# Performance work log

Hardware: AMD Instinct MI355X
Metric: run time of the kernel (lower is better)

Reference implementation:

```python
import jax, jax.numpy as jnp
import numpy as np

N, E, G = 50000, 800000, 500
F_IN, H_DIM, L, NH, HD, OUT = 74, 256, 4, 8, 32, 1
SLOPE, EPS = 0.2, 1e-5


def setup_inputs() -> dict:
    key = jax.random.key(0)
    ks = jax.random.split(key, 24)
    rn = lambda k, s, sc: jax.random.normal(k, s, jnp.float32) * sc
    inp = {
        "x": jax.random.normal(ks[0], (N, F_IN), jnp.float32),
        "edge_index": jax.random.randint(ks[1], (2, E), 0, N),
        "batch": jnp.sort(jax.random.randint(ks[2], (N,), 0, G)),
        "in_w": rn(ks[3], (F_IN, H_DIM), 1.0 / np.sqrt(F_IN)),
        "in_b": jnp.zeros((H_DIM,), jnp.float32),
        "wl": rn(ks[4], (L, H_DIM, H_DIM), 1.0 / np.sqrt(H_DIM)),
        "wl_b": jnp.zeros((L, H_DIM), jnp.float32),
        "wr": rn(ks[5], (L, H_DIM, H_DIM), 1.0 / np.sqrt(H_DIM)),
        "wr_b": jnp.zeros((L, H_DIM), jnp.float32),
        "att": rn(ks[6], (L, NH, HD), 1.0 / np.sqrt(HD)),
        "gat_b": jnp.zeros((L, H_DIM), jnp.float32),
        "ln_g": jnp.ones((L, H_DIM), jnp.float32),
        "ln_b": jnp.zeros((L, H_DIM), jnp.float32),
        "out_w": rn(ks[7], (H_DIM, H_DIM), 1.0 / np.sqrt(H_DIM)),
        "out_b": jnp.zeros((H_DIM,), jnp.float32),
        "p1_w": rn(ks[8], (H_DIM, H_DIM // 2), 1.0 / np.sqrt(H_DIM)),
        "p1_b": jnp.zeros((H_DIM // 2,), jnp.float32),
        "bn1_g": jnp.ones((H_DIM // 2,), jnp.float32),
        "bn1_b": jnp.zeros((H_DIM // 2,), jnp.float32),
        "p2_w": rn(ks[9], (H_DIM // 2, H_DIM // 4), 1.0 / np.sqrt(H_DIM // 2)),
        "p2_b": jnp.zeros((H_DIM // 4,), jnp.float32),
        "bn2_g": jnp.ones((H_DIM // 4,), jnp.float32),
        "bn2_b": jnp.zeros((H_DIM // 4,), jnp.float32),
        "p3_w": rn(ks[10], (H_DIM // 4, OUT), 1.0 / np.sqrt(H_DIM // 4)),
        "p3_b": jnp.zeros((OUT,), jnp.float32),
    }
    return inp


def _layer_norm(x, g, b):
    m = x.mean(-1, keepdims=True)
    v = ((x - m) ** 2).mean(-1, keepdims=True)
    return (x - m) * jax.lax.rsqrt(v + EPS) * g + b


def _batch_norm(x, g, b):
    m = x.mean(0)
    v = ((x - m) ** 2).mean(0)
    return (x - m) * jax.lax.rsqrt(v + EPS) * g + b


def _gatv2(h, src, dst, wl, wl_b, wr, wr_b, att, bias, n):
    xl = (h @ wl + wl_b).reshape(n, NH, HD)  # source transform
    xr = (h @ wr + wr_b).reshape(n, NH, HD)  # target transform
    e = jax.nn.leaky_relu(xl[src] + xr[dst], SLOPE)      # [E, H, D]
    score = jnp.einsum('ehd,hd->eh', e, att)             # [E, H]
    smax = jax.ops.segment_max(score, dst, num_segments=n)
    num = jnp.exp(score - smax[dst])
    den = jax.ops.segment_sum(num, dst, num_segments=n)
    alpha = num / (den[dst] + 1e-16)                     # segment softmax per dst
    out = jax.ops.segment_sum(xl[src] * alpha[:, :, None], dst, num_segments=n)
    return out.reshape(n, NH * HD) + bias


def reference(x, edge_index, batch, in_w, in_b, wl, wl_b, wr, wr_b, att, gat_b,
              ln_g, ln_b, out_w, out_b, p1_w, p1_b, bn1_g, bn1_b,
              p2_w, p2_b, bn2_g, bn2_b, p3_w, p3_b):
    n = x.shape[0]
    loops = jnp.arange(n)
    src = jnp.concatenate([edge_index[0], loops])  # add self-loops (PyG default)
    dst = jnp.concatenate([edge_index[1], loops])
    h = x @ in_w + in_b
    for i in range(L):
        res = h
        g = _gatv2(h, src, dst, wl[i], wl_b[i], wr[i], wr_b[i], att[i], gat_b[i], n)
        if i > 0:
            g = g + res
        h = jax.nn.relu(_layer_norm(g, ln_g[i], ln_b[i]))
    h = h @ out_w + out_b
    cnt = jax.ops.segment_sum(jnp.ones((n,), h.dtype), batch, num_segments=G)
    gr = jax.ops.segment_sum(h, batch, num_segments=G) / jnp.maximum(cnt, 1.0)[:, None]
    z = jax.nn.relu(_batch_norm(gr @ p1_w + p1_b, bn1_g, bn1_b))
    z = jax.nn.relu(_batch_norm(z @ p2_w + p2_b, bn2_g, bn2_b))
    return z @ p3_w + p3_b
```

## Files before the change

### kernel.cpp

```cpp
#include <hip/hip_runtime.h>
#include <hip/hip_bf16.h>

#define F_IN   74
#define KPAD   96
#define HDIM   256
#define NHEAD  8
#define HEADD  32
#define NLAYER 4
#define SLOPE  0.2f
#define EPSN   1e-5f
#define LOG2E  1.44269504088896f

typedef __attribute__((ext_vector_type(8))) short bf16x8;
typedef __attribute__((ext_vector_type(4))) float f32x4;
typedef __attribute__((ext_vector_type(2))) float f32x2;

__device__ __forceinline__ float bf2f(unsigned short u){
  union { unsigned int i; float f; } x; x.i = ((unsigned int)u) << 16; return x.f;
}
__device__ __forceinline__ unsigned short f2bf(float f){
  union { float f; unsigned int i; } x; x.f = f;
  unsigned int u = x.i;
  return (unsigned short)((u + 0x7FFFu + ((u >> 16) & 1u)) >> 16);
}
__device__ __forceinline__ f32x2 bfpair(unsigned int u){
  union { unsigned int i; float f; } lo, hi;
  lo.i = u << 16; hi.i = u & 0xffff0000u;
  return (f32x2){lo.f, hi.f};
}
__device__ __forceinline__ float dpp_sum8(float p){
  int t;
  t = __builtin_amdgcn_update_dpp(0, __float_as_int(p), 0xB1, 0xF, 0xF, true);
  p += __int_as_float(t);
  t = __builtin_amdgcn_update_dpp(0, __float_as_int(p), 0x4E, 0xF, 0xF, true);
  p += __int_as_float(t);
  t = __builtin_amdgcn_update_dpp(0, __float_as_int(p), 0x141, 0xF, 0xF, true);
  p += __int_as_float(t);
  return p;
}
__device__ __forceinline__ float dpp_sum16(float p){
  int t;
  p = dpp_sum8(p);
  t = __builtin_amdgcn_update_dpp(0, __float_as_int(p), 0x140, 0xF, 0xF, true);
  p += __int_as_float(t);
  return p;
}

#define GLOAD16(g, s) __builtin_amdgcn_global_load_lds( \
  (const __attribute__((address_space(1))) void*)(g), \
  (__attribute__((address_space(3))) void*)(s), 16, 0, 0)

__global__ void k_hist(const int* __restrict__ dst, int* __restrict__ deg, int e){
  int i = blockIdx.x * 256 + threadIdx.x;
  if (i < e) atomicAdd(&deg[dst[i]], 1);
}

__global__ __launch_bounds__(256) void k_scan1(const int* __restrict__ deg,
    int* __restrict__ rowp, int* __restrict__ bsum, int n){
  __shared__ int wsum[4];
  const int tid = threadIdx.x, lane = tid & 63, wid = tid >> 6;
  const int i = blockIdx.x * 256 + tid;
  int v = (i < n) ? (deg[i] + 1) : 0;
  int xv = v;
  #pragma unroll
  for (int off = 1; off < 64; off <<= 1){
    int t = __shfl_up(xv, off);
    if (lane >= off) xv += t;
  }
  if (lane == 63) wsum[wid] = xv;
  __syncthreads();
  int woff = 0, total = 0;
  #pragma unroll
  for (int w = 0; w < 4; ++w){
    int s = wsum[w];
    total += s;
    if (w < wid) woff += s;
  }
  if (i < n) rowp[i] = woff + xv - v;
  if (tid == 0) bsum[blockIdx.x] = total;
}
__global__ __launch_bounds__(256) void k_scan2(const int* __restrict__ bsum,
    int* __restrict__ boff, int nb){
  __shared__ int wsum[4];
  const int tid = threadIdx.x, lane = tid & 63, wid = tid >> 6;
  int v = (tid < nb) ? bsum[tid] : 0;
  int xv = v;
  #pragma unroll
  for (int off = 1; off < 64; off <<= 1){
    int t = __shfl_up(xv, off);
    if (lane >= off) xv += t;
  }
  if (lane == 63) wsum[wid] = xv;
  __syncthreads();
  int woff = 0, total = 0;
  #pragma unroll
  for (int w = 0; w < 4; ++w){
    int s = wsum[w];
    total += s;
    if (w < wid) woff += s;
  }
  if (tid <= nb) boff[tid] = woff + xv - v;
  if (tid == 0) boff[nb] = total;
}
__global__ void k_scan3(int* __restrict__ rowp, int* __restrict__ cur,
                        const int* __restrict__ boff, int n, int nb){
  int i = blockIdx.x * 256 + threadIdx.x;
  if (i < n){
    int v = rowp[i] + boff[blockIdx.x];
    rowp[i] = v;
    cur[i] = v;
  }
  if (i == 0) rowp[n] = boff[nb];
}

__global__ void k_fill2(const int* __restrict__ src, const int* __restrict__ dst,
                        int* __restrict__ cur, unsigned int* __restrict__ csr,
                        int e, int n){
  int i = blockIdx.x * 256 + threadIdx.x;
  if (i < e){
    int p = atomicAdd(&cur[dst[i]], 1);
    csr[p] = ((unsigned int)src[i]) << 10;
  } else if (i < e + n){
    int v = i - e;
    int p = atomicAdd(&cur[v], 1);
    csr[p] = ((unsigned int)v) << 10;
  }
}

__global__ __launch_bounds__(256) void k_prep(
    const float* __restrict__ wl, const float* __restrict__ wr,
    const float* __restrict__ out_w, const float* __restrict__ in_w,
    const float* __restrict__ wl_b, const float* __restrict__ wr_b,
    const float* __restrict__ x,
    unsigned short* __restrict__ WtLR, unsigned short* __restrict__ WtO,
    unsigned short* __restrict__ WtI, float* __restrict__ bconc,
    unsigned short* __restrict__ xb, int n)
{
  const int b = blockIdx.x;
  const int tid = threadIdx.x;
  if (b < 576){
    __shared__ float tile[32][33];
    const float* Wm;
    unsigned short* Wo;
    int rem, colbase;
    if (b < 512){
      const int matset = b >> 8;
      const int mat = (b >> 6) & 3;
      rem = b & 63;
      const float* srcw = matset ? wr : wl;
      Wm = srcw + (size_t)mat * HDIM * HDIM;
      Wo = WtLR + (size_t)mat * 512 * HDIM;
      colbase = matset * 256;
    } else {
      rem = b - 512;
      Wm = out_w; Wo = WtO; colbase = 0;
    }
    const int c0 = (rem & 7) * 32, r0 = (rem >> 3) * 32;
    const int tx = tid & 31, ty = tid >> 5;
    #pragma unroll
    for (int i = 0; i < 32; i += 8)
      tile[ty + i][tx] = Wm[(size_t)(r0 + ty + i) * HDIM + c0 + tx];
    __syncthreads();
    #pragma unroll
    for (int i = 0; i < 32; i += 8){
      const int col = colbase + c0 + ty + i;
      const int k   = r0 + tx;
      const int cb = col >> 4, ks = k >> 5;
      const int lf = (col & 15) | (((k >> 3) & 3) << 4);
      Wo[((size_t)(cb * 8 + ks) * 64 + lf) * 8 + (k & 7)] = f2bf(tile[tx][ty + i]);
    }
  } else if (b < 672){
    int idx = (b - 576) * 256 + tid;
    int c = idx / KPAD, k = idx - c * KPAD;
    float v = (k < F_IN) ? in_w[(size_t)k * HDIM + c] : 0.f;
    WtI[idx] = f2bf(v);
  } else if (b < 680){
    int i = (b - 672) * 256 + tid;
    if (i < NLAYER * 512){
      int layer = i >> 9, c = i & 511;
      bconc[i] = (c < 256) ? wl_b[layer * 256 + c] : wr_b[layer * 256 + (c - 256)];
    }
  } else {
    int idx = (b - 680) * 256 + tid;
    if (idx < n * KPAD){
      int row = idx / KPAD, k = idx - row * KPAD;
      float v = (k < F_IN) ? x[(size_t)row * F_IN + k] : 0.f;
      xb[idx] = f2bf(v);
    }
  }
}

__global__ __launch_bounds__(256) void k_inproj_mfma(
    const unsigned short* __restrict__ xb, const unsigned short* __restrict__ Wt,
    const float* __restrict__ bias, unsigned short* __restrict__ C, int M)
{
  const int l = threadIdx.x & 63;
  const int w = threadIdx.x >> 6;
  const int wm = w >> 1, wn = w & 1;
  const int row0 = blockIdx.x * 128;
  const int col0 = blockIdx.y * 128;

  f32x4 acc[4][4];
  #pragma unroll
  for (int i = 0; i < 4; ++i)
    #pragma unroll
    for (int j = 0; j < 4; ++j) acc[i][j] = (f32x4){0.f, 0.f, 0.f, 0.f};

  #pragma unroll
  for (int kk = 0; kk < 3; ++kk){
    const int kof = kk * 32 + (l >> 4) * 8;
    bf16x8 af[4], bfr[4];
    #pragma unroll
    for (int mi = 0; mi < 4; ++mi){
      int row = row0 + wm * 64 + mi * 16 + (l & 15);
      if (row > M - 1) row = M - 1;
      af[mi] = *(const bf16x8*)(xb + (size_t)row * KPAD + kof);
    }
    #pragma unroll
    for (int ni = 0; ni < 4; ++ni){
      const int col = col0 + wn * 64 + ni * 16 + (l & 15);
      bfr[ni] = *(const bf16x8*)(Wt + (size_t)col * KPAD + kof);
    }
    #pragma unroll
    for (int mi = 0; mi < 4; ++mi)
      #pragma unroll
      for (int ni = 0; ni < 4; ++ni)
        acc[mi][ni] = __builtin_amdgcn_mfma_f32_16x16x32_bf16(
            af[mi], bfr[ni], acc[mi][ni], 0, 0, 0);
  }

  #pragma unroll
  for (int mi = 0; mi < 4; ++mi){
    #pragma unroll
    for (int ni = 0; ni < 4; ++ni){
      const int col = col0 + wn * 64 + ni * 16 + (l & 15);
      const float bv = bias[col];
      #pragma unroll
      for (int r = 0; r < 4; ++r){
        const int row = row0 + wm * 64 + mi * 16 + (l >> 4) * 4 + r;
        if (row < M) C[(size_t)row * HDIM + col] = f2bf(acc[mi][ni][r] + bv);
      }
    }
  }
}

__global__ __launch_bounds__(256) void k_gemm_mfma(
    const unsigned short* __restrict__ A, const unsigned short* __restrict__ Wt,
    const float* __restrict__ bias, unsigned short* __restrict__ C, int M, int ldc)
{
  __shared__ unsigned short As[2][128 * 64];
  const int tid = threadIdx.x;
  const int l   = tid & 63;
  const int w   = tid >> 6;
  const int wm  = w >> 1, wn = w & 1;
  const int row0 = blockIdx.x * 128;
  const int col0 = blockIdx.y * 128;

  const int srow   = l >> 3;
  const int schunk = l & 7;

  f32x4 acc[4][4];
  #pragma unroll
  for (int i = 0; i < 4; ++i)
    #pragma unroll
    for (int j = 0; j < 4; ++j) acc[i][j] = (f32x4){0.f, 0.f, 0.f, 0.f};

  auto stageA = [&](int buf, int k0){
    #pragma unroll
    for (int i = 0; i < 4; ++i){
      const int rloc = w * 32 + i * 8 + srow;
      const int sw   = (schunk ^ (rloc & 7)) * 16;
      int ra = row0 + rloc; if (ra > M - 1) ra = M - 1;
      const char* srcA = (const char*)(A + (size_t)ra * HDIM + k0) + sw;
      GLOAD16(srcA, &As[buf][(w * 32 + i * 8) * 64]);
    }
  };

  const unsigned short* Bf = Wt + ((size_t)(col0 / 16 + wn * 4) * 8 * 64 + l) * 8;

  stageA(0, 0);
  asm volatile("s_waitcnt vmcnt(0)" ::: "memory");
  __builtin_amdgcn_s_barrier();
  int buf = 0;
  #pragma unroll
  for (int t = 0; t < 4; ++t){
    bf16x8 bfr[2][4];
    #pragma unroll
    for (int kk = 0; kk < 2; ++kk)
      #pragma unroll
      for (int ni = 0; ni < 4; ++ni)
        bfr[kk][ni] = *(const bf16x8*)(Bf + ((size_t)ni * 8 + (t * 2 + kk)) * 64 * 8);
    if (t < 3) stageA(buf ^ 1, (t + 1) * 64);
    #pragma unroll
    for (int kk = 0; kk < 2; ++kk){
      bf16x8 af[4];
      #pragma unroll
      for (int mi = 0; mi < 4; ++mi){
        const int row = wm * 64 + mi * 16 + (l & 15);
        const int tt  = (kk * 4 + (l >> 4)) ^ (row & 7);
        af[mi] = *(const bf16x8*)((const char*)&As[buf][0] + row * 128 + tt * 16);
      }
      #pragma unroll
      for (int mi = 0; mi < 4; ++mi)
        #pragma unroll
        for (int ni = 0; ni < 4; ++ni)
          acc[mi][ni] = __builtin_amdgcn_mfma_f32_16x16x32_bf16(
              af[mi], bfr[kk][ni], acc[mi][ni], 0, 0, 0);
    }
    if (t < 3){
      asm volatile("s_waitcnt vmcnt(0)" ::: "memory");
      __builtin_amdgcn_s_barrier();
      buf ^= 1;
    }
  }

  #pragma unroll
  for (int mi = 0; mi < 4; ++mi){
    #pragma unroll
    for (int ni = 0; ni < 4; ++ni){
      const int col = col0 + wn * 64 + ni * 16 + (l & 15);
      const float bv = bias[col];
      #pragma unroll
      for (int r = 0; r < 4; ++r){
        const int row = row0 + wm * 64 + mi * 16 + (l >> 4) * 4 + r;
        if (row < M) C[(size_t)row * ldc + col] = f2bf(acc[mi][ni][r] + bv);
      }
    }
  }
}

__global__ __launch_bounds__(256) void k_gat(
    const unsigned short* __restrict__ xlr,
    const int* __restrict__ rp, const unsigned int* __restrict__ csr,
    const float* __restrict__ att, const float* __restrict__ gb,
    const float* __restrict__ lg, const float* __restrict__ lb,
    const unsigned short* __restrict__ hold, unsigned short* __restrict__ hnew,
    int n, int use_res)
{
  const int node = blockIdx.x * 4 + (threadIdx.x >> 6);
  if (node >= n) return;
  const int lane = threadIdx.x & 63;
  const int elem = lane << 2;
  const int head = lane >> 3;
  float4 attv = *(const float4*)(att + head * HEADD + (elem & 31));
  const f32x2 av01 = {attv.x * LOG2E, attv.y * LOG2E};
  const f32x2 av23 = {attv.z * LOG2E, attv.w * LOG2E};
  uint2 ur = *(const uint2*)(xlr + (size_t)node * 512 + 256 + elem);
  const f32x2 r01 = bfpair(ur.x), r23 = bfpair(ur.y);

  const char* xbase = (const char*)xlr + (elem << 1);

  f32x2 a01 = {0.f, 0.f}, a23 = {0.f, 0.f};
  float l = 0.f;

  auto edgeq = [&](uint2 uu, f32x2& x01, f32x2& x23)->float{
    x01 = bfpair(uu.x); x23 = bfpair(uu.y);
    f32x2 t01 = x01 + r01, t23 = x23 + r23;
    f32x2 m01 = __builtin_elementwise_max(t01, t01 * SLOPE);
    f32x2 m23 = __builtin_elementwise_max(t23, t23 * SLOPE);
    f32x2 d = m01 * av01 + m23 * av23;
    float p = dpp_sum8(d.x + d.y);
    return exp2f(p);
  };

  const int e0 = rp[node], e1 = rp[node + 1];
  int e = e0;
  for (; e + 4 <= e1; e += 4){
    unsigned int o0 = csr[e], o1 = csr[e + 1], o2 = csr[e + 2], o3 = csr[e + 3];
    uint2 u0 = *(const uint2*)(xbase + o0);
    uint2 u1 = *(const uint2*)(xbase + o1);
    uint2 u2 = *(const uint2*)(xbase + o2);
    uint2 u3 = *(const uint2*)(xbase + o3);
    f32x2 x01, x23;
    float q0 = edgeq(u0, x01, x23);
    a01 += q0 * x01; a23 += q0 * x23;
    float q1 = edgeq(u1, x01, x23);
    a01 += q1 * x01; a23 += q1 * x23;
    float q2 = edgeq(u2, x01, x23);
    a01 += q2 * x01; a23 += q2 * x23;
    float q3 = edgeq(u3, x01, x23);
    a01 += q3 * x01; a23 += q3 * x23;
    l += (q0 + q1) + (q2 + q3);
  }
  for (; e < e1; ++e){
    unsigned int o = csr[e];
    uint2 u = *(const uint2*)(xbase + o);
    f32x2 x01, x23;
    float q = edgeq(u, x01, x23);
    l += q;
    a01 += q * x01; a23 += q * x23;
  }

  const float inv = 1.f / l;
  const size_t base = (size_t)node * HDIM + elem;
  float f0 = a01.x * inv + gb[elem + 0];
  float f1 = a01.y * inv + gb[elem + 1];
  float f2 = a23.x * inv + gb[elem + 2];
  float f3 = a23.y * inv + gb[elem + 3];
  if (use_res){
    ushort4 hv = *(const ushort4*)(hold + base);
    f0 += bf2f(hv.x); f1 += bf2f(hv.y); f2 += bf2f(hv.z); f3 += bf2f(hv.w);
  }
  float s = f0 + f1 + f2 + f3;
  s = dpp_sum16(s);
  s += __shfl_xor(s, 16);
  s += __shfl_xor(s, 32);
  const float mean = s * (1.f / HDIM);
  float d0 = f0 - mean, d1 = f1 - mean, d2 = f2 - mean, d3 = f3 - mean;
  float q = d0 * d0 + d1 * d1 + d2 * d2 + d3 * d3;
  q = dpp_sum16(q);
  q += __shfl_xor(q, 16);
  q += __shfl_xor(q, 32);
  const float rs = rsqrtf(q * (1.f / HDIM) + EPSN);
  float o0 = d0 * rs * lg[elem + 0] + lb[elem + 0]; o0 = o0 > 0.f ? o0 : 0.f;
  float o1 = d1 * rs * lg[elem + 1] + lb[elem + 1]; o1 = o1 > 0.f ? o1 : 0.f;
  float o2 = d2 * rs * lg[elem + 2] + lb[elem + 2]; o2 = o2 > 0.f ? o2 : 0.f;
  float o3 = d3 * rs * lg[elem + 3] + lb[elem + 3]; o3 = o3 > 0.f ? o3 : 0.f;
  ushort4 st; st.x = f2bf(o0); st.y = f2bf(o1); st.z = f2bf(o2); st.w = f2bf(o3);
  *(ushort4*)(hnew + base) = st;
}

__global__ __launch_bounds__(256) void k_pool2(
    const unsigned short* __restrict__ ho, const int* __restrict__ batch,
    float* __restrict__ gr, int n)
{
  const int g = blockIdx.x;
  int lo = 0, hi = n;
  while (lo < hi){ int mid = (lo + hi) >> 1; if (batch[mid] < g) lo = mid + 1; else hi = mid; }
  const int s = lo;
  hi = n;
  while (lo < hi){ int mid = (lo + hi) >> 1; if (batch[mid] < g + 1) lo = mid + 1; else hi = mid; }
  const int e = lo;
  const int j = threadIdx.x;
  float acc = 0.f;
  for (int i = s; i < e; ++i) acc += bf2f(ho[(size_t)i * HDIM + j]);
  int c = e - s; if (c < 1) c = 1;
  gr[(size_t)g * HDIM + j] = acc / (float)c;
}

__global__ void k_fc(const float* __restrict__ in, const float* __restrict__ w,
                     const float* __restrict__ b, float* __restrict__ out,
                     int kin, int kout){
  __shared__ float s[256];
  int g = blockIdx.x, j = threadIdx.x;
  for (int k = j; k < kin; k += blockDim.x) s[k] = in[(size_t)g * kin + k];
  __syncthreads();
  float a = b[j];
  for (int k = 0; k < kin; ++k) a = fmaf(s[k], w[k * kout + j], a);
  out[(size_t)g * kout + j] = a;
}

__global__ __launch_bounds__(256) void k_bn(float* __restrict__ z,
    const float* __restrict__ gam, const float* __restrict__ bet, int g_, int c_){
  const int c = blockIdx.x;
  float s = 0.f, s2 = 0.f;
  for (int r = threadIdx.x; r < g_; r += 256){
    float v = z[(size_t)r * c_ + c];
    s += v; s2 += v * v;
  }
  #pragma unroll
  for (int off = 1; off < 64; off <<= 1){ s += __shfl_xor(s, off); s2 += __shfl_xor(s2, off); }
  __shared__ float sw[4], sw2[4];
  __shared__ float smean, srstd;
  int lane = threadIdx.x & 63, wid = threadIdx.x >> 6;
  if (lane == 0){ sw[wid] = s; sw2[wid] = s2; }
  __syncthreads();
  if (threadIdx.x == 0){
    float ts = sw[0] + sw[1] + sw[2] + sw[3];
    float ts2 = sw2[0] + sw2[1] + sw2[2] + sw2[3];
    float mm = ts / g_;
    float vv = ts2 / g_ - mm * mm;
    smean = mm; srstd = rsqrtf(vv + EPSN);
  }
  __syncthreads();
  const float mm = smean, rs = srstd, gg = gam[c], bb = bet[c];
  for (int r = threadIdx.x; r < g_; r += 256){
    float v = (z[(size_t)r * c_ + c] - mm) * rs * gg + bb;
    z[(size_t)r * c_ + c] = v > 0.f ? v : 0.f;
  }
}

__global__ __launch_bounds__(256) void k_out(const float* __restrict__ z,
    const float* __restrict__ w, const float* __restrict__ b,
    float* __restrict__ out, int g_){
  int g = blockIdx.x * 4 + (threadIdx.x >> 6);
  if (g >= g_) return;
  int lane = threadIdx.x & 63;
  float v = z[(size_t)g * 64 + lane] * w[lane];
  #pragma unroll
  for (int off = 1; off < 64; off <<= 1) v += __shfl_xor(v, off);
  if (lane == 0) out[g] = v + b[0];
}

extern "C" void kernel_launch(void* const* d_in, const int* in_sizes, int n_in,
                              void* d_out, int out_size, void* d_ws, size_t ws_size,
                              hipStream_t stream)
{
  const float* x     = (const float*)d_in[0];
  const int*   ei    = (const int*)  d_in[1];
  const int*   batch = (const int*)  d_in[2];
  const float* in_w  = (const float*)d_in[3];
  const float* in_b  = (const float*)d_in[4];
  const float* wl    = (const float*)d_in[5];
  const float* wl_b  = (const float*)d_in[6];
  const float* wr    = (const float*)d_in[7];
  const float* wr_b  = (const float*)d_in[8];
  const float* att   = (const float*)d_in[9];
  const float* gat_b = (const float*)d_in[10];
  const float* ln_g  = (const float*)d_in[11];
  const float* ln_b  = (const float*)d_in[12];
  const float* out_w = (const float*)d_in[13];
  const float* out_b = (const float*)d_in[14];
  const float* p1_w  = (const float*)d_in[15];
  const float* p1_b  = (const float*)d_in[16];
  const float* bn1_g = (const float*)d_in[17];
  const float* bn1_b = (const float*)d_in[18];
  const float* p2_w  = (const float*)d_in[19];
  const float* p2_b  = (const float*)d_in[20];
  const float* bn2_g = (const float*)d_in[21];
  const float* bn2_b = (const float*)d_in[22];
  const float* p3_w  = (const float*)d_in[23];
  const float* p3_b  = (const float*)d_in[24];

  const int n = in_sizes[0] / F_IN;
  const int e = in_sizes[1] / 2;
  const int g = out_size;
  const int nb = (n + 255) / 256;

  char* p = (char*)d_ws;
  auto take = [&](size_t bytes)->char*{
    char* q = p; p += ((bytes + 255) & ~(size_t)255); return q;
  };
  unsigned short* hA   = (unsigned short*)take((size_t)n * HDIM * 2);
  unsigned short* hB   = (unsigned short*)take((size_t)n * HDIM * 2);
  unsigned short* xlr  = (unsigned short*)take((size_t)n * 512 * 2);
  unsigned short* WtLR = (unsigned short*)take((size_t)NLAYER * 512 * HDIM * 2);
  unsigned short* WtO  = (unsigned short*)take((size_t)HDIM * HDIM * 2);
  unsigned short* WtI  = (unsigned short*)take((size_t)HDIM * KPAD * 2);
  float* bconc = (float*)take((size_t)NLAYER * 512 * 4);
  int*   deg   = (int*)take((size_t)n * 4);
  int*   rowp  = (int*)take((size_t)(n + 1) * 4);
  int*   cur   = (int*)take((size_t)n * 4);
  unsigned int* csr = (unsigned int*)take((size_t)(e + n) * 4);
  int*   bsum  = (int*)take((size_t)(nb + 1) * 4);
  int*   boff  = (int*)take((size_t)(nb + 1) * 4);
  float* gr    = (float*)take((size_t)g * HDIM * 4);
  float* z1    = (float*)take((size_t)g * 128 * 4);
  float* z2    = (float*)take((size_t)g * 64 * 4);
  unsigned short* xb = xlr;
  (void)ws_size; (void)n_in;

  hipMemsetAsync(deg, 0, (size_t)n * 4, stream);
  k_hist<<<(e + 255) / 256, 256, 0, stream>>>(ei + e, deg, e);
  k_scan1<<<nb, 256, 0, stream>>>(deg, rowp, bsum, n);
  k_scan2<<<1, 256, 0, stream>>>(bsum, boff, nb);
  k_scan3<<<nb, 256, 0, stream>>>(rowp, cur, boff, n, nb);
  k_fill2<<<(e + n + 255) / 256, 256, 0, stream>>>(ei, ei + e, cur, csr, e, n);

  const int xconv_blocks = (n * KPAD + 255) / 256;
  k_prep<<<680 + xconv_blocks, 256, 0, stream>>>(
      wl, wr, out_w, in_w, wl_b, wr_b, x, WtLR, WtO, WtI, bconc, xb, n);

  k_inproj_mfma<<<dim3((n + 127) / 128, 2), 256, 0, stream>>>(xb, WtI, in_b, hA, n);

  unsigned short* hcur = hA;
  unsigned short* hnext = hB;
  for (int i = 0; i < NLAYER; ++i){
    k_gemm_mfma<<<dim3((n + 127) / 128, 4), 256, 0, stream>>>(
        hcur, WtLR + (size_t)i * 512 * HDIM, bconc + i * 512, xlr, n, 512);
    k_gat<<<(n + 3) / 4, 256, 0, stream>>>(xlr, rowp, csr,
        att + (size_t)i * NHEAD * HEADD, gat_b + i * HDIM,
        ln_g + i * HDIM, ln_b + i * HDIM, hcur, hnext, n, i > 0 ? 1 : 0);
    unsigned short* t = hcur; hcur = hnext; hnext = t;
  }
  k_gemm_mfma<<<dim3((n + 127) / 128, 2), 256, 0, stream>>>(
      hcur, WtO, out_b, hnext, n, HDIM);

  k_pool2<<<g, 256, 0, stream>>>(hnext, batch, gr, n);

  k_fc<<<g, 128, 0, stream>>>(gr, p1_w, p1_b, z1, HDIM, 128);
  k_bn<<<128, 256, 0, stream>>>(z1, bn1_g, bn1_b, g, 128);
  k_fc<<<g, 64, 0, stream>>>(z1, p2_w, p2_b, z2, 128, 64);
  k_bn<<<64, 256, 0, stream>>>(z2, bn2_g, bn2_b, g, 64);
  k_out<<<(g + 3) / 4, 256, 0, stream>>>(z2, p3_w, p3_b, (float*)d_out, g);
}
```

Measured before the change: 662.9 us.

## Load full K-panel of A into LDS once instead of double-buffered K stages

The GEMM kernel now stages the entire 128x256 bf16 A tile (64 KB) into shared memory up front with one wait and barrier. It then runs all eight K-steps of MFMA with no further barriers, replacing the four-stage double-buffered pipeline. This removes the per-stage barrier and waitcnt stalls. In exchange the LDS footprint doubles, which may lower occupancy, and global load latency is no longer overlapped with compute inside a block.

```diff
diff --git a/kernel.cpp b/kernel.cpp
--- a/kernel.cpp
+++ b/kernel.cpp
@@ -248,7 +248,7 @@
     const unsigned short* __restrict__ A, const unsigned short* __restrict__ Wt,
     const float* __restrict__ bias, unsigned short* __restrict__ C, int M, int ldc)
 {
-  __shared__ unsigned short As[2][128 * 64];
+  __shared__ unsigned short As[128 * 256];
   const int tid = threadIdx.x;
   const int l   = tid & 63;
   const int w   = tid >> 6;
@@ -256,8 +256,21 @@
   const int row0 = blockIdx.x * 128;
   const int col0 = blockIdx.y * 128;
 
-  const int srow   = l >> 3;
-  const int schunk = l & 7;
+  {
+    const int lrow = l >> 5;
+    const int lchunk = l & 31;
+    #pragma unroll
+    for (int i = 0; i < 16; ++i){
+      const int rbase = i * 8 + w * 2;
+      const int rloc  = rbase + lrow;
+      const int sw    = (lchunk ^ (rloc & 7)) * 16;
+      int ra = row0 + rloc; if (ra > M - 1) ra = M - 1;
+      const char* srcA = (const char*)(A + (size_t)ra * HDIM) + sw;
+      GLOAD16(srcA, &As[rbase * 256]);
+    }
+  }
+
+  const unsigned short* Bf = Wt + ((size_t)(col0 / 16 + wn * 4) * 8 * 64 + l) * 8;
 
   f32x4 acc[4][4];
   #pragma unroll
@@ -265,53 +278,27 @@
     #pragma unroll
     for (int j = 0; j < 4; ++j) acc[i][j] = (f32x4){0.f, 0.f, 0.f, 0.f};
 
-  auto stageA = [&](int buf, int k0){
-    #pragma unroll
-    for (int i = 0; i < 4; ++i){
-      const int rloc = w * 32 + i * 8 + srow;
-      const int sw   = (schunk ^ (rloc & 7)) * 16;
-      int ra = row0 + rloc; if (ra > M - 1) ra = M - 1;
-      const char* srcA = (const char*)(A + (size_t)ra * HDIM + k0) + sw;
-      GLOAD16(srcA, &As[buf][(w * 32 + i * 8) * 64]);
-    }
-  };
-
-  const unsigned short* Bf = Wt + ((size_t)(col0 / 16 + wn * 4) * 8 * 64 + l) * 8;
-
-  stageA(0, 0);
   asm volatile("s_waitcnt vmcnt(0)" ::: "memory");
   __builtin_amdgcn_s_barrier();
-  int buf = 0;
-  #pragma unroll
-  for (int t = 0; t < 4; ++t){
-    bf16x8 bfr[2][4];
-    #pragma unroll
-    for (int kk = 0; kk < 2; ++kk)
+
+  #pragma unroll
+  for (int ks = 0; ks < 8; ++ks){
+    bf16x8 bfr[4], af[4];
+    #pragma unroll
+    for (int ni = 0; ni < 4; ++ni)
+      bfr[ni] = *(const bf16x8*)(Bf + ((size_t)ni * 8 + ks) * 64 * 8);
+    #pragma unroll
+    for (int mi = 0; mi < 4; ++mi){
+      const int row = wm * 64 + mi * 16 + (l & 15);
+      const int c   = (ks * 4 + (l >> 4)) ^ (row & 7);
+      af[mi] = *(const bf16x8*)((const char*)As + row * 512 + c * 16);
+    }
+    #pragma unroll
+    for (int mi = 0; mi < 4; ++mi)
       #pragma unroll
       for (int ni = 0; ni < 4; ++ni)
-        bfr[kk][ni] = *(const bf16x8*)(Bf + ((size_t)ni * 8 + (t * 2 + kk)) * 64 * 8);
-    if (t < 3) stageA(buf ^ 1, (t + 1) * 64);
-    #pragma unroll
-    for (int kk = 0; kk < 2; ++kk){
-      bf16x8 af[4];
-      #pragma unroll
-      for (int mi = 0; mi < 4; ++mi){
-        const int row = wm * 64 + mi * 16 + (l & 15);
-        const int tt  = (kk * 4 + (l >> 4)) ^ (row & 7);
-        af[mi] = *(const bf16x8*)((const char*)&As[buf][0] + row * 128 + tt * 16);
-      }
-      #pragma unroll
-      for (int mi = 0; mi < 4; ++mi)
-        #pragma unroll
-        for (int ni = 0; ni < 4; ++ni)
-          acc[mi][ni] = __builtin_amdgcn_mfma_f32_16x16x32_bf16(
-              af[mi], bfr[kk][ni], acc[mi][ni], 0, 0, 0);
-    }
-    if (t < 3){
-      asm volatile("s_waitcnt vmcnt(0)" ::: "memory");
-      __builtin_amdgcn_s_barrier();
-      buf ^= 1;
-    }
+        acc[mi][ni] = __builtin_amdgcn_mfma_f32_16x16x32_bf16(
+            af[mi], bfr[ni], acc[mi][ni], 0, 0, 0);
   }
 
   #pragma unroll
```

New measurement: 706.6 us. 1.07x slower.
